# Kernel optimization log

Hardware: AMD Instinct MI355X
Metric: run time of the kernel (lower is better)

## Reference

```python
import jax, jax.numpy as jnp
import numpy as np

B, T, C = 16, 512, 1024
D, K, W = 4096, 128, 8


def _scatter_topk(a, k, use_values):
    """Top-k along last axis; return dense array with top-k values (or 1.0) scattered, zeros elsewhere."""
    shp = a.shape
    a2 = a.reshape(-1, shp[-1])
    vals, idx = jax.lax.top_k(a2, k)
    rows = jnp.arange(a2.shape[0])[:, None]
    src = vals if use_values else jnp.ones_like(vals)
    return jnp.zeros_like(a2).at[rows, idx].set(src).reshape(shp)


def _window_topk(x, k, window_size):
    # x: (B, T, D)
    b, t, d = x.shape
    stride = max(1, window_size // 2)
    if stride >= t:
        num_windows, pad, t_pad = 1, 0, t
    else:
        num_windows = (t - window_size) // stride + 1
        required = (num_windows - 1) * stride + window_size
        pad = max(0, required - t)
        t_pad = t + pad
    if pad > 0:
        x = jnp.pad(x, ((0, 0), (0, pad), (0, 0)))
    starts = jnp.arange(num_windows) * stride                      # (NW,)
    tidx = starts[:, None] + jnp.arange(window_size)               # (NW, W)
    x_windows = x[:, tidx, :]                                      # (B, NW, W, D)
    window_sums = x_windows.sum(axis=2)                            # (B, NW, D)
    mask_windows = _scatter_topk(window_sums, k, use_values=False)  # (B, NW, D)
    votes = (x_windows * mask_windows[:, :, None, :]).reshape(b, num_windows * window_size, d)
    feature_votes = jnp.zeros((b, t_pad, d), x.dtype).at[:, tidx.reshape(-1)].add(votes)
    mask_combined = _scatter_topk(feature_votes, k, use_values=False)  # (B, Tp, D)
    x_sparse = x * mask_combined
    return x_sparse[:, :t - 0, :] if pad > 0 else x_sparse


def setup_inputs() -> dict:
    key = jax.random.key(0)
    ks = jax.random.split(key, 4)
    x_ssl = jax.random.normal(ks[0], (B, T, C), jnp.float32)
    W_dec = jax.random.normal(ks[1], (C, D), jnp.float32)
    W_dec = W_dec / jnp.linalg.norm(W_dec, axis=0, keepdims=True)
    W_enc = W_dec.T                                                # tied init, as in module
    W1 = jax.random.normal(ks[2], (256, D), jnp.float32) * (1.0 / np.sqrt(D))
    W2 = jax.random.normal(ks[3], (2, 256), jnp.float32) * (1.0 / np.sqrt(256))
    return dict(
        x_ssl=x_ssl, W_enc=W_enc, b_enc=jnp.zeros((D,), jnp.float32),
        W_dec=W_dec, b_dec=jnp.zeros((C,), jnp.float32),
        ln_g=jnp.ones((D,), jnp.float32), ln_b=jnp.zeros((D,), jnp.float32),
        W1=W1, b1=jnp.zeros((256,), jnp.float32),
        W2=W2, b2=jnp.zeros((2,), jnp.float32),
    )


def reference(x_ssl, W_enc, b_enc, W_dec, b_dec, ln_g, ln_b, W1, b1, W2, b2):
    b, t, c = x_ssl.shape
    x_flat = x_ssl.reshape(b * t, c)
    # SAE encode with window top-k (window_size=8 > 1 path)
    pre = jnp.einsum('nc,dc->nd', x_flat - b_dec, W_enc) + b_enc
    post_relu = jax.nn.relu(pre).reshape(b, t, -1)                 # (B, T, D)
    encoded = _window_topk(post_relu, K, W)                        # (B, T, D)
    encoded_flat = encoded.reshape(b * t, -1)
    # SAE decode + reconstruction loss
    x_recon = jnp.einsum('nd,cd->nc', encoded_flat, W_dec) + b_dec
    sae_loss = jnp.mean((x_recon - x_flat) ** 2)
    # classifier on pooled sparse features (dropout is inference no-op)
    pooled = encoded.mean(axis=1)                                  # (B, D) == AdaptiveAvgPool1d(1)
    mu = pooled.mean(axis=-1, keepdims=True)
    var = pooled.var(axis=-1, keepdims=True)
    ln = (pooled - mu) / jnp.sqrt(var + 1e-5) * ln_g + ln_b
    h = jax.nn.relu(ln @ W1.T + b1)
    logits = h @ W2.T + b2
    log_probs = jax.nn.log_softmax(logits, axis=-1)
    return log_probs, sae_loss
```

## Files before the change

### kernel.cpp

```cpp
#include <hip/hip_runtime.h>

#define BB   16
#define TT   512
#define CC   1024
#define DD   4096
#define NN   (BB*TT)
#define NWIN 127
#define KTOP 128

typedef __attribute__((ext_vector_type(8))) short short8;
typedef _Float16 half8 __attribute__((ext_vector_type(8)));
typedef __attribute__((ext_vector_type(4))) float f32x4;

__device__ __forceinline__ unsigned short f2bf(float f) {
    unsigned u = __float_as_uint(f);
    unsigned r = (u + 0x7fffu + ((u >> 16) & 1u)) >> 16;
    return (unsigned short)r;
}
__device__ __forceinline__ float bf2f(unsigned x) {
    return __uint_as_float((x & 0xffffu) << 16);
}
__device__ __forceinline__ unsigned short f2h(float f) {
    union { _Float16 h; unsigned short u; } c;
    c.h = (_Float16)f;
    return c.u;
}
__device__ __forceinline__ unsigned tokey(float f) {
    unsigned u = __float_as_uint(f);
    return (u & 0x80000000u) ? ~u : (u | 0x80000000u);
}
__device__ __forceinline__ void async_lds16(const void* g, void* l) {
    __builtin_amdgcn_global_load_lds((const __attribute__((address_space(1))) void*)g,
                                     (__attribute__((address_space(3))) void*)l, 16, 0, 0);
}

__device__ __forceinline__ unsigned wave_prefix_incl(unsigned v) {
    int lane = threadIdx.x & 63;
#pragma unroll
    for (int off = 1; off < 64; off <<= 1) {
        unsigned n = __shfl_up(v, off, 64);
        if (lane >= off) v += n;
    }
    return v;
}
__device__ __forceinline__ unsigned wave_suffix_incl(unsigned v) {
    int lane = threadIdx.x & 63;
#pragma unroll
    for (int off = 1; off < 64; off <<= 1) {
        unsigned n = __shfl_down(v, off, 64);
        if (lane + off < 64) v += n;
    }
    return v;
}

__device__ __forceinline__ unsigned select_top128(const unsigned* keys,
                                                  unsigned* hist, unsigned* shx) {
    const int tid = threadIdx.x, wid = tid >> 6, lane = tid & 63;
    const unsigned ZKEY = 0x80000000u;
    unsigned cpos = 0, cz = 0;
#pragma unroll
    for (int i = 0; i < 16; ++i) {
        cpos += (keys[i] > ZKEY);
        cz   += (keys[i] == ZKEY);
    }
    unsigned ppos = wave_prefix_incl(cpos);
    unsigned pz   = wave_prefix_incl(cz);
    if (lane == 63) { shx[wid] = ppos; shx[4 + wid] = pz; }
    __syncthreads();
    unsigned nz = shx[0] + shx[1] + shx[2] + shx[3];
    unsigned selbits = 0u;
    if (nz <= KTOP) {
        unsigned need = KTOP - nz;
        unsigned zr = pz - cz;
        if (wid > 0) zr += shx[4];
        if (wid > 1) zr += shx[5];
        if (wid > 2) zr += shx[6];
#pragma unroll
        for (int i = 0; i < 16; ++i) {
            bool sel = (keys[i] > ZKEY) || (keys[i] == ZKEY && zr < need);
            if (keys[i] == ZKEY) ++zr;
            selbits |= (sel ? 1u : 0u) << i;
        }
        return selbits;
    }
    unsigned k2[16];
#pragma unroll
    for (int i = 0; i < 16; ++i) k2[i] = (keys[i] > ZKEY) ? keys[i] : 0u;
    unsigned prefix = 0u, pmask = 0u, Kr = KTOP;
    for (int shift = 24; shift >= 0; shift -= 8) {
        hist[tid] = 0u; hist[256 + tid] = 0u; hist[512 + tid] = 0u; hist[768 + tid] = 0u;
        __syncthreads();
        unsigned* h = hist + (wid << 8);
#pragma unroll
        for (int i = 0; i < 16; ++i)
            if (k2[i] && (k2[i] & pmask) == prefix) atomicAdd(&h[(k2[i] >> shift) & 255u], 1u);
        __syncthreads();
        unsigned v = hist[tid] + hist[256 + tid] + hist[512 + tid] + hist[768 + tid];
        unsigned s = wave_suffix_incl(v);
        if (lane == 0) shx[wid] = s;
        __syncthreads();
        unsigned stot = s;
        if (wid == 0) stot += shx[1] + shx[2] + shx[3];
        else if (wid == 1) stot += shx[2] + shx[3];
        else if (wid == 2) stot += shx[3];
        unsigned above = stot - v;
        if (stot >= Kr && above < Kr) { shx[8] = (unsigned)tid; shx[9] = Kr - above; }
        __syncthreads();
        prefix |= shx[8] << shift;
        pmask |= 0xFFu << shift;
        Kr = shx[9];
    }
    unsigned T = prefix, need = Kr;
    unsigned ce = 0;
#pragma unroll
    for (int i = 0; i < 16; ++i) ce += (k2[i] == T);
    unsigned pe = wave_prefix_incl(ce);
    __syncthreads();
    if (lane == 63) shx[4 + wid] = pe;
    __syncthreads();
    unsigned er = pe - ce;
    if (wid > 0) er += shx[4];
    if (wid > 1) er += shx[5];
    if (wid > 2) er += shx[6];
#pragma unroll
    for (int i = 0; i < 16; ++i) {
        bool sel = (k2[i] > T) || (k2[i] == T && er < need);
        if (k2[i] == T) ++er;
        selbits |= (sel ? 1u : 0u) << i;
    }
    return selbits;
}

__global__ __launch_bounds__(256) void k_convert(const float* __restrict__ in,
                                                 unsigned short* __restrict__ out,
                                                 size_t n4) {
    size_t i = (size_t)blockIdx.x * 256 + threadIdx.x;
    if (i >= n4) return;
    float4 v = ((const float4*)in)[i];
    uint2 o;
    o.x = (unsigned)f2bf(v.x) | ((unsigned)f2bf(v.y) << 16);
    o.y = (unsigned)f2bf(v.z) | ((unsigned)f2bf(v.w) << 16);
    ((uint2*)out)[i] = o;
}

__global__ __launch_bounds__(256) void k_convert_f16(const float* __restrict__ in,
                                                     unsigned short* __restrict__ out,
                                                     const float* __restrict__ bias,
                                                     size_t n4) {
    size_t i = (size_t)blockIdx.x * 256 + threadIdx.x;
    if (i >= n4) return;
    float4 v = ((const float4*)in)[i];
    if (bias) {
        size_t c = (i * 4) & (CC - 1);
        v.x -= bias[c]; v.y -= bias[c + 1]; v.z -= bias[c + 2]; v.w -= bias[c + 3];
    }
    uint2 o;
    o.x = (unsigned)f2h(v.x) | ((unsigned)f2h(v.y) << 16);
    o.y = (unsigned)f2h(v.z) | ((unsigned)f2h(v.w) << 16);
    ((uint2*)out)[i] = o;
}

__device__ __forceinline__ void stage_tile_swz(const unsigned short* gbase, size_t ldk,
                                               unsigned short* lds, int wave, int lane) {
    const int sub = lane >> 3;
    const int cj  = (lane & 7) ^ sub;
#pragma unroll
    for (int i = 0; i < 4; ++i) {
        int n = wave * 4 + i;
        int r = n * 8 + sub;
        async_lds16(gbase + (size_t)r * ldk + cj * 8, lds + n * 512);
    }
}

__global__ __launch_bounds__(256) void k_gemm_enc_f16(const unsigned short* __restrict__ Ah,
                                                      const unsigned short* __restrict__ Bh,
                                                      const float* __restrict__ bias,
                                                      float* __restrict__ Cout,
                                                      float* __restrict__ gsum,
                                                      int Ndim, int Kdim) {
    __shared__ __align__(16) unsigned short At[128 * 64];
    __shared__ __align__(16) unsigned short Bt[128 * 64];
    const int tid = threadIdx.x, wave = tid >> 6, lane = tid & 63;
    const int bm = blockIdx.y * 128, bn = blockIdx.x * 128;
    const int wm = (wave >> 1) * 64, wn = (wave & 1) * 64;
    const int rA = lane & 15, q8 = (lane >> 4) * 8, rp7 = rA & 7;
    f32x4 acc[4][4] = {};
    for (int k0 = 0; k0 < Kdim; k0 += 64) {
        __syncthreads();
        stage_tile_swz(Ah + (size_t)bm * Kdim + k0, Kdim, At, wave, lane);
        stage_tile_swz(Bh + (size_t)bn * Kdim + k0, Kdim, Bt, wave, lane);
        __syncthreads();
#pragma unroll
        for (int kk = 0; kk < 64; kk += 32) {
            const int sc = ((((kk + q8) >> 3) ^ rp7) << 3);
            half8 a[4], b[4];
#pragma unroll
            for (int mt = 0; mt < 4; ++mt) a[mt] = *(const half8*)(At + (wm + mt * 16 + rA) * 64 + sc);
#pragma unroll
            for (int nt = 0; nt < 4; ++nt) b[nt] = *(const half8*)(Bt + (wn + nt * 16 + rA) * 64 + sc);
#pragma unroll
            for (int mt = 0; mt < 4; ++mt)
#pragma unroll
                for (int nt = 0; nt < 4; ++nt)
                    acc[mt][nt] = __builtin_amdgcn_mfma_f32_16x16x32_f16(a[mt], b[nt], acc[mt][nt], 0, 0, 0);
        }
    }
    const int cl = lane & 15, qr = (lane >> 4) * 4;
#pragma unroll
    for (int nt = 0; nt < 4; ++nt) {
        int col = bn + wn + nt * 16 + cl;
        float bv = bias[col];
#pragma unroll
        for (int mt = 0; mt < 4; ++mt) {
            int row0 = bm + wm + mt * 16 + qr;
            float gs = 0.f;
#pragma unroll
            for (int r = 0; r < 4; ++r) {
                float v = acc[mt][nt][r] + bv;
                v = v > 0.f ? v : 0.f;
                gs += v;
                Cout[(size_t)(row0 + r) * Ndim + col] = v;
            }
            if (gsum) gsum[(size_t)(row0 >> 2) * Ndim + col] = gs;
        }
    }
}

__global__ __launch_bounds__(256) void k_gemm_recon(const unsigned short* __restrict__ A,
                                                    size_t lda,
                                                    const unsigned short* __restrict__ Bm,
                                                    const float* __restrict__ bdec,
                                                    const float* __restrict__ X,
                                                    float* __restrict__ sae,
                                                    int Ndim, int Kdim) {
    __shared__ __align__(16) unsigned short At[128 * 64];
    __shared__ __align__(16) unsigned short Bt[128 * 64];
    __shared__ float red[256];
    const int tid = threadIdx.x, wave = tid >> 6, lane = tid & 63;
    const int bm = blockIdx.y * 128, bn = blockIdx.x * 128;
    const int wm = (wave >> 1) * 64, wn = (wave & 1) * 64;
    const int rA = lane & 15, q8 = (lane >> 4) * 8, rp7 = rA & 7;
    f32x4 acc[4][4] = {};
    for (int k0 = 0; k0 < Kdim; k0 += 64) {
        __syncthreads();
        stage_tile_swz(A + (size_t)bm * lda + k0, lda, At, wave, lane);
        stage_tile_swz(Bm + (size_t)bn * Kdim + k0, Kdim, Bt, wave, lane);
        __syncthreads();
#pragma unroll
        for (int kk = 0; kk < 64; kk += 32) {
            const int sc = ((((kk + q8) >> 3) ^ rp7) << 3);
            short8 a[4], b[4];
#pragma unroll
            for (int mt = 0; mt < 4; ++mt) a[mt] = *(const short8*)(At + (wm + mt * 16 + rA) * 64 + sc);
#pragma unroll
            for (int nt = 0; nt < 4; ++nt) b[nt] = *(const short8*)(Bt + (wn + nt * 16 + rA) * 64 + sc);
#pragma unroll
            for (int mt = 0; mt < 4; ++mt)
#pragma unroll
                for (int nt = 0; nt < 4; ++nt)
                    acc[mt][nt] = __builtin_amdgcn_mfma_f32_16x16x32_bf16(a[mt], b[nt], acc[mt][nt], 0, 0, 0);
        }
    }
    const int cl = lane & 15, qr = (lane >> 4) * 4;
    float lsum = 0.f;
#pragma unroll
    for (int nt = 0; nt < 4; ++nt) {
        int col = bn + wn + nt * 16 + cl;
        float bv = bdec[col];
#pragma unroll
        for (int mt = 0; mt < 4; ++mt) {
            int row0 = bm + wm + mt * 16 + qr;
#pragma unroll
            for (int r = 0; r < 4; ++r) {
                float v = acc[mt][nt][r] + bv - X[(size_t)(row0 + r) * Ndim + col];
                lsum += v * v;
            }
        }
    }
    red[tid] = lsum;
    __syncthreads();
    for (int s = 128; s > 0; s >>= 1) { if (tid < s) red[tid] += red[tid + s]; __syncthreads(); }
    if (tid == 0) atomicAdd(sae, red[0]);
}

__global__ __launch_bounds__(256) void k_winsum_g(const float* __restrict__ gsum,
                                                  unsigned* __restrict__ wmask) {
    __shared__ unsigned hist[1024];
    __shared__ unsigned shx[16];
    __shared__ unsigned short halves[256];
    const int tid = threadIdx.x, w = blockIdx.x, b = blockIdx.y;
    const float* g0 = gsum + ((size_t)(b * 128 + w)) * DD + tid * 16;
    const float* g1 = g0 + DD;
    unsigned keys[16];
#pragma unroll
    for (int q = 0; q < 4; ++q) {
        float4 u = *(const float4*)(g0 + q * 4);
        float4 v = *(const float4*)(g1 + q * 4);
        keys[q * 4 + 0] = tokey(u.x + v.x);
        keys[q * 4 + 1] = tokey(u.y + v.y);
        keys[q * 4 + 2] = tokey(u.z + v.z);
        keys[q * 4 + 3] = tokey(u.w + v.w);
    }
    unsigned selbits = select_top128(keys, hist, shx);
    halves[tid] = (unsigned short)selbits;
    __syncthreads();
    if (tid < 128)
        wmask[(size_t)(b * NWIN + w) * 128 + tid] =
            (unsigned)halves[2 * tid] | ((unsigned)halves[2 * tid + 1] << 16);
}

__global__ __launch_bounds__(256) void k_winsum_p(const float* __restrict__ post,
                                                  unsigned* __restrict__ wmask) {
    __shared__ unsigned hist[1024];
    __shared__ unsigned shx[16];
    __shared__ unsigned short halves[256];
    const int tid = threadIdx.x, w = blockIdx.x, b = blockIdx.y;
    const float* base = post + (size_t)(b * TT + w * 4) * DD + tid * 16;
    float s[16] = {};
#pragma unroll
    for (int j = 0; j < 8; ++j) {
        const float* rp = base + (size_t)j * DD;
#pragma unroll
        for (int q = 0; q < 4; ++q) {
            float4 u = *(const float4*)(rp + q * 4);
            s[q * 4 + 0] += u.x; s[q * 4 + 1] += u.y; s[q * 4 + 2] += u.z; s[q * 4 + 3] += u.w;
        }
    }
    unsigned keys[16];
#pragma unroll
    for (int i = 0; i < 16; ++i) keys[i] = tokey(s[i]);
    unsigned selbits = select_top128(keys, hist, shx);
    halves[tid] = (unsigned short)selbits;
    __syncthreads();
    if (tid < 128)
        wmask[(size_t)(b * NWIN + w) * 128 + tid] =
            (unsigned)halves[2 * tid] | ((unsigned)halves[2 * tid + 1] << 16);
}

__global__ __launch_bounds__(256) void k_votes(float* __restrict__ post,
                                               const unsigned* __restrict__ wmask,
                                               float* __restrict__ pooled) {
    __shared__ unsigned hist[1024];
    __shared__ unsigned shx[16];
    const int tid = threadIdx.x, t = blockIdx.x, b = blockIdx.y;
    float* rp = post + (size_t)(b * TT + t) * DD;
    int w1 = t >> 2, w0 = w1 - 1;
    unsigned mw0 = 0u, mw1 = 0u;
    if (w0 >= 0)        mw0 = wmask[(size_t)(b * NWIN + w0) * 128 + (tid >> 1)];
    if (w1 <= NWIN - 1) mw1 = wmask[(size_t)(b * NWIN + w1) * 128 + (tid >> 1)];
    const int bbase = (tid & 1) * 16;
    float vals[16];
    unsigned keys[16];
#pragma unroll
    for (int q = 0; q < 4; ++q) {
        float4 u = *(const float4*)(rp + tid * 16 + q * 4);
        vals[q * 4 + 0] = u.x; vals[q * 4 + 1] = u.y; vals[q * 4 + 2] = u.z; vals[q * 4 + 3] = u.w;
    }
#pragma unroll
    for (int i = 0; i < 16; ++i) {
        float cov = (float)(((mw0 >> (bbase + i)) & 1u) + ((mw1 >> (bbase + i)) & 1u));
        keys[i] = tokey(vals[i] * cov);
    }
    unsigned selbits = select_top128(keys, hist, shx);
    unsigned packed[8];
#pragma unroll
    for (int i = 0; i < 16; i += 2) {
        float v0 = (selbits >> i) & 1u ? vals[i] : 0.f;
        float v1 = (selbits >> (i + 1)) & 1u ? vals[i + 1] : 0.f;
        if (v0 != 0.f) atomicAdd(&pooled[(size_t)b * DD + tid * 16 + i], v0);
        if (v1 != 0.f) atomicAdd(&pooled[(size_t)b * DD + tid * 16 + i + 1], v1);
        packed[i >> 1] = (unsigned)f2bf(v0) | ((unsigned)f2bf(v1) << 16);
    }
    unsigned short* op = (unsigned short*)rp;
    *(uint4*)(op + tid * 16)     = *(uint4*)&packed[0];
    *(uint4*)(op + tid * 16 + 8) = *(uint4*)&packed[4];
}

__device__ __forceinline__ float block_sum(float v, float* red) {
    const int tid = threadIdx.x;
    red[tid] = v;
    __syncthreads();
    for (int s = 128; s > 0; s >>= 1) { if (tid < s) red[tid] += red[tid + s]; __syncthreads(); }
    float r = red[0];
    __syncthreads();
    return r;
}

__global__ __launch_bounds__(256) void k_head_ln(const float* __restrict__ pooled,
                                                 const float* __restrict__ lng,
                                                 const float* __restrict__ lnb,
                                                 float* __restrict__ lnout) {
    __shared__ float red[256];
    const int b = blockIdx.x, tid = threadIdx.x;
    float pv[16];
    float s = 0.f;
#pragma unroll
    for (int q = 0; q < 4; ++q) {
        float4 u = *(const float4*)(pooled + (size_t)b * DD + tid * 16 + q * 4);
        pv[q * 4 + 0] = u.x * (1.f / TT); pv[q * 4 + 1] = u.y * (1.f / TT);
        pv[q * 4 + 2] = u.z * (1.f / TT); pv[q * 4 + 3] = u.w * (1.f / TT);
        s += pv[q * 4 + 0] + pv[q * 4 + 1] + pv[q * 4 + 2] + pv[q * 4 + 3];
    }
    float mean = block_sum(s, red) * (1.f / (float)DD);
    float vs = 0.f;
#pragma unroll
    for (int i = 0; i < 16; ++i) { float c = pv[i] - mean; vs += c * c; }
    float var = block_sum(vs, red) * (1.f / (float)DD);
    float inv = rsqrtf(var + 1e-5f);
#pragma unroll
    for (int q = 0; q < 4; ++q) {
        float4 g = *(const float4*)(lng + tid * 16 + q * 4);
        float4 bb = *(const float4*)(lnb + tid * 16 + q * 4);
        float4 o;
        o.x = (pv[q * 4 + 0] - mean) * inv * g.x + bb.x;
        o.y = (pv[q * 4 + 1] - mean) * inv * g.y + bb.y;
        o.z = (pv[q * 4 + 2] - mean) * inv * g.z + bb.z;
        o.w = (pv[q * 4 + 3] - mean) * inv * g.w + bb.w;
        *(float4*)(lnout + (size_t)b * DD + tid * 16 + q * 4) = o;
    }
}

__global__ __launch_bounds__(256) void k_head_mlp(const float* __restrict__ lnout,
                                                  const float* __restrict__ W1,
                                                  const float* __restrict__ b1,
                                                  float* __restrict__ h) {
    const int gw = (blockIdx.x * 256 + threadIdx.x) >> 6;
    const int lane = threadIdx.x & 63;
    const int b = gw >> 8, row = gw & 255;
    const float* lp = lnout + (size_t)b * DD;
    const float* wr = W1 + (size_t)row * DD;
    float a = 0.f;
#pragma unroll
    for (int k = 0; k < DD / 64; ++k)
        a += lp[lane + 64 * k] * wr[lane + 64 * k];
#pragma unroll
    for (int off = 32; off > 0; off >>= 1) a += __shfl_down(a, off, 64);
    if (lane == 0) h[b * 256 + row] = fmaxf(a + b1[row], 0.f);
}

__global__ __launch_bounds__(256) void k_head_out(const float* __restrict__ h,
                                                  const float* __restrict__ W2,
                                                  const float* __restrict__ b2,
                                                  const float* __restrict__ sae,
                                                  float* __restrict__ out) {
    __shared__ float red[256];
    const int b = blockIdx.x, tid = threadIdx.x;
    float hv = h[b * 256 + tid];
    float l0 = block_sum(hv * W2[tid], red) + b2[0];
    float l1 = block_sum(hv * W2[256 + tid], red) + b2[1];
    if (tid == 0) {
        float m = fmaxf(l0, l1);
        float lse = m + logf(expf(l0 - m) + expf(l1 - m));
        out[2 * b] = l0 - lse;
        out[2 * b + 1] = l1 - lse;
        if (b == 0) out[32] = sae[0] * (1.f / (float)((size_t)NN * CC));
    }
}

extern "C" void kernel_launch(void* const* d_in, const int* in_sizes, int n_in,
                              void* d_out, int out_size, void* d_ws, size_t ws_size,
                              hipStream_t stream) {
    const float* x    = (const float*)d_in[0];
    const float* Wenc = (const float*)d_in[1];
    const float* benc = (const float*)d_in[2];
    const float* Wdec = (const float*)d_in[3];
    const float* bdec = (const float*)d_in[4];
    const float* lng  = (const float*)d_in[5];
    const float* lnb  = (const float*)d_in[6];
    const float* W1   = (const float*)d_in[7];
    const float* b1   = (const float*)d_in[8];
    const float* W2   = (const float*)d_in[9];
    const float* b2   = (const float*)d_in[10];
    float* out = (float*)d_out;

    char* ws = (char*)d_ws;
    float*          post  = (float*)(ws + 0);
    unsigned short* xh16  = (unsigned short*)(ws + 134217728);
    unsigned short* scr   = (unsigned short*)(ws + 150994944);
    unsigned short* wh16  = (unsigned short*)(ws + 167772160);
    unsigned short* wdecb = (unsigned short*)(ws + 184549376);
    unsigned*       wmask = (unsigned*)(ws + 192937984);
    float*          pooled= (float*)(ws + 193978368);
    float*          sae   = (float*)(ws + 194240512);
    float*          gsum  = (float*)(ws + 194240768);
    const bool use_gsum = ws_size >= (size_t)194240768 + 33554432;
    float* gptr = use_gsum ? gsum : nullptr;
    float* lnout = (float*)xh16;
    float* hbuf  = (float*)scr;

    hipMemsetAsync(pooled, 0, 262144 + 256, stream);

    k_convert_f16<<<dim3((NN * CC) / 1024), 256, 0, stream>>>(x, xh16, bdec, (size_t)NN * CC / 4);
    k_convert_f16<<<dim3((DD * CC) / 1024), 256, 0, stream>>>(Wenc, wh16, nullptr, (size_t)DD * CC / 4);
    k_convert<<<dim3((CC * DD) / 1024), 256, 0, stream>>>(Wdec, wdecb, (size_t)CC * DD / 4);

    k_gemm_enc_f16<<<dim3(DD / 128, NN / 128), 256, 0, stream>>>(xh16, wh16, benc, post, gptr, DD, CC);
    if (use_gsum)
        k_winsum_g<<<dim3(NWIN, BB), 256, 0, stream>>>(gsum, wmask);
    else
        k_winsum_p<<<dim3(NWIN, BB), 256, 0, stream>>>(post, wmask);
    k_votes<<<dim3(TT, BB), 256, 0, stream>>>(post, wmask, pooled);
    k_gemm_recon<<<dim3(CC / 128, NN / 128), 256, 0, stream>>>((const unsigned short*)post, (size_t)2 * DD,
                                                               wdecb, bdec, x, sae, CC, DD);
    k_head_ln<<<dim3(BB), 256, 0, stream>>>(pooled, lng, lnb, lnout);
    k_head_mlp<<<dim3(1024), 256, 0, stream>>>(lnout, W1, b1, hbuf);
    k_head_out<<<dim3(BB), 256, 0, stream>>>(hbuf, W2, b2, sae, out);
}
```

Measured before the change: 468.8 us.

## Fuse conversions, stage encoder epilogue through LDS, double-buffer recon GEMM

```diff
diff --git a/kernel.cpp b/kernel.cpp
--- a/kernel.cpp
+++ b/kernel.cpp
@@ -131,33 +131,38 @@
     return selbits;
 }
 
-__global__ __launch_bounds__(256) void k_convert(const float* __restrict__ in,
-                                                 unsigned short* __restrict__ out,
-                                                 size_t n4) {
-    size_t i = (size_t)blockIdx.x * 256 + threadIdx.x;
-    if (i >= n4) return;
-    float4 v = ((const float4*)in)[i];
-    uint2 o;
-    o.x = (unsigned)f2bf(v.x) | ((unsigned)f2bf(v.y) << 16);
-    o.y = (unsigned)f2bf(v.z) | ((unsigned)f2bf(v.w) << 16);
-    ((uint2*)out)[i] = o;
-}
-
-__global__ __launch_bounds__(256) void k_convert_f16(const float* __restrict__ in,
-                                                     unsigned short* __restrict__ out,
-                                                     const float* __restrict__ bias,
-                                                     size_t n4) {
-    size_t i = (size_t)blockIdx.x * 256 + threadIdx.x;
-    if (i >= n4) return;
-    float4 v = ((const float4*)in)[i];
-    if (bias) {
+__global__ __launch_bounds__(256) void k_convert_all(const float* __restrict__ x,
+                                                     const float* __restrict__ Wenc,
+                                                     const float* __restrict__ Wdec,
+                                                     const float* __restrict__ bdec,
+                                                     unsigned short* __restrict__ xh,
+                                                     unsigned short* __restrict__ wh,
+                                                     unsigned short* __restrict__ wdb) {
+    const int bid = blockIdx.x;
+    if (bid < 8192) {
+        size_t i = (size_t)bid * 256 + threadIdx.x;
+        float4 v = ((const float4*)x)[i];
         size_t c = (i * 4) & (CC - 1);
-        v.x -= bias[c]; v.y -= bias[c + 1]; v.z -= bias[c + 2]; v.w -= bias[c + 3];
-    }
-    uint2 o;
-    o.x = (unsigned)f2h(v.x) | ((unsigned)f2h(v.y) << 16);
-    o.y = (unsigned)f2h(v.z) | ((unsigned)f2h(v.w) << 16);
-    ((uint2*)out)[i] = o;
+        v.x -= bdec[c]; v.y -= bdec[c + 1]; v.z -= bdec[c + 2]; v.w -= bdec[c + 3];
+        uint2 o;
+        o.x = (unsigned)f2h(v.x) | ((unsigned)f2h(v.y) << 16);
+        o.y = (unsigned)f2h(v.z) | ((unsigned)f2h(v.w) << 16);
+        ((uint2*)xh)[i] = o;
+    } else if (bid < 12288) {
+        size_t i = (size_t)(bid - 8192) * 256 + threadIdx.x;
+        float4 v = ((const float4*)Wenc)[i];
+        uint2 o;
+        o.x = (unsigned)f2h(v.x) | ((unsigned)f2h(v.y) << 16);
+        o.y = (unsigned)f2h(v.z) | ((unsigned)f2h(v.w) << 16);
+        ((uint2*)wh)[i] = o;
+    } else {
+        size_t i = (size_t)(bid - 12288) * 256 + threadIdx.x;
+        float4 v = ((const float4*)Wdec)[i];
+        uint2 o;
+        o.x = (unsigned)f2bf(v.x) | ((unsigned)f2bf(v.y) << 16);
+        o.y = (unsigned)f2bf(v.z) | ((unsigned)f2bf(v.w) << 16);
+        ((uint2*)wdb)[i] = o;
+    }
 }
 
 __device__ __forceinline__ void stage_tile_swz(const unsigned short* gbase, size_t ldk,
@@ -178,12 +183,15 @@
                                                       float* __restrict__ Cout,
                                                       float* __restrict__ gsum,
                                                       int Ndim, int Kdim) {
-    __shared__ __align__(16) unsigned short At[128 * 64];
-    __shared__ __align__(16) unsigned short Bt[128 * 64];
+    __shared__ __align__(16) unsigned short smem[2 * 128 * 64];
+    unsigned short* At = smem;
+    unsigned short* Bt = smem + 128 * 64;
+    float* cbuf = (float*)smem;
     const int tid = threadIdx.x, wave = tid >> 6, lane = tid & 63;
     const int bm = blockIdx.y * 128, bn = blockIdx.x * 128;
     const int wm = (wave >> 1) * 64, wn = (wave & 1) * 64;
     const int rA = lane & 15, q8 = (lane >> 4) * 8, rp7 = rA & 7;
+    const int q = lane >> 4, qr = q * 4, cl = lane & 15;
     f32x4 acc[4][4] = {};
     for (int k0 = 0; k0 < Kdim; k0 += 64) {
         __syncthreads();
@@ -205,23 +213,46 @@
                     acc[mt][nt] = __builtin_amdgcn_mfma_f32_16x16x32_f16(a[mt], b[nt], acc[mt][nt], 0, 0, 0);
         }
     }
-    const int cl = lane & 15, qr = (lane >> 4) * 4;
-#pragma unroll
-    for (int nt = 0; nt < 4; ++nt) {
-        int col = bn + wn + nt * 16 + cl;
-        float bv = bias[col];
-#pragma unroll
-        for (int mt = 0; mt < 4; ++mt) {
-            int row0 = bm + wm + mt * 16 + qr;
-            float gs = 0.f;
-#pragma unroll
-            for (int r = 0; r < 4; ++r) {
-                float v = acc[mt][nt][r] + bv;
-                v = v > 0.f ? v : 0.f;
-                gs += v;
-                Cout[(size_t)(row0 + r) * Ndim + col] = v;
+    float bv[4];
+#pragma unroll
+    for (int nt = 0; nt < 4; ++nt) bv[nt] = bias[bn + wn + nt * 16 + cl];
+#pragma unroll
+    for (int p = 0; p < 2; ++p) {
+        __syncthreads();
+        if ((wave >> 1) == p) {
+#pragma unroll
+            for (int nt = 0; nt < 4; ++nt) {
+                int lc = wn + nt * 16 + cl;
+                int pcb = (lc >> 2) ^ (q << 1);
+#pragma unroll
+                for (int mt = 0; mt < 4; ++mt) {
+#pragma unroll
+                    for (int r = 0; r < 4; ++r) {
+                        int lr = mt * 16 + qr + r;
+                        float v = acc[mt][nt][r] + bv[nt];
+                        v = v > 0.f ? v : 0.f;
+                        cbuf[lr * 128 + pcb * 4 + (lc & 3)] = v;
+                    }
+                }
             }
-            if (gsum) gsum[(size_t)(row0 >> 2) * Ndim + col] = gs;
+        }
+        __syncthreads();
+#pragma unroll
+        for (int i = 0; i < 2; ++i) {
+            int gidx = i * 256 + tid;
+            int grow = gidx >> 5;
+            int colg = gidx & 31;
+            float4 s = make_float4(0.f, 0.f, 0.f, 0.f);
+#pragma unroll
+            for (int j = 0; j < 4; ++j) {
+                int lr = grow * 4 + j;
+                int pcr = colg ^ (((lr >> 2) & 3) << 1);
+                float4 v = *(const float4*)&cbuf[lr * 128 + pcr * 4];
+                s.x += v.x; s.y += v.y; s.z += v.z; s.w += v.w;
+                *(float4*)&Cout[(size_t)(bm + p * 64 + lr) * Ndim + bn + colg * 4] = v;
+            }
+            if (gsum)
+                *(float4*)&gsum[(size_t)((bm >> 2) + p * 16 + grow) * Ndim + bn + colg * 4] = s;
         }
     }
 }
@@ -233,33 +264,38 @@
                                                     const float* __restrict__ X,
                                                     float* __restrict__ sae,
                                                     int Ndim, int Kdim) {
-    __shared__ __align__(16) unsigned short At[128 * 64];
-    __shared__ __align__(16) unsigned short Bt[128 * 64];
+    __shared__ __align__(16) unsigned short At[2][128 * 64];
+    __shared__ __align__(16) unsigned short Bt[2][128 * 64];
     __shared__ float red[256];
     const int tid = threadIdx.x, wave = tid >> 6, lane = tid & 63;
     const int bm = blockIdx.y * 128, bn = blockIdx.x * 128;
     const int wm = (wave >> 1) * 64, wn = (wave & 1) * 64;
     const int rA = lane & 15, q8 = (lane >> 4) * 8, rp7 = rA & 7;
     f32x4 acc[4][4] = {};
+    stage_tile_swz(A + (size_t)bm * lda, lda, At[0], wave, lane);
+    stage_tile_swz(Bm + (size_t)bn * Kdim, Kdim, Bt[0], wave, lane);
+    __syncthreads();
     for (int k0 = 0; k0 < Kdim; k0 += 64) {
-        __syncthreads();
-        stage_tile_swz(A + (size_t)bm * lda + k0, lda, At, wave, lane);
-        stage_tile_swz(Bm + (size_t)bn * Kdim + k0, Kdim, Bt, wave, lane);
-        __syncthreads();
+        const int cur = (k0 >> 6) & 1;
+        if (k0 + 64 < Kdim) {
+            stage_tile_swz(A + (size_t)bm * lda + k0 + 64, lda, At[cur ^ 1], wave, lane);
+            stage_tile_swz(Bm + (size_t)bn * Kdim + k0 + 64, Kdim, Bt[cur ^ 1], wave, lane);
+        }
 #pragma unroll
         for (int kk = 0; kk < 64; kk += 32) {
             const int sc = ((((kk + q8) >> 3) ^ rp7) << 3);
             short8 a[4], b[4];
 #pragma unroll
-            for (int mt = 0; mt < 4; ++mt) a[mt] = *(const short8*)(At + (wm + mt * 16 + rA) * 64 + sc);
-#pragma unroll
-            for (int nt = 0; nt < 4; ++nt) b[nt] = *(const short8*)(Bt + (wn + nt * 16 + rA) * 64 + sc);
+            for (int mt = 0; mt < 4; ++mt) a[mt] = *(const short8*)(At[cur] + (wm + mt * 16 + rA) * 64 + sc);
+#pragma unroll
+            for (int nt = 0; nt < 4; ++nt) b[nt] = *(const short8*)(Bt[cur] + (wn + nt * 16 + rA) * 64 + sc);
 #pragma unroll
             for (int mt = 0; mt < 4; ++mt)
 #pragma unroll
                 for (int nt = 0; nt < 4; ++nt)
                     acc[mt][nt] = __builtin_amdgcn_mfma_f32_16x16x32_bf16(a[mt], b[nt], acc[mt][nt], 0, 0, 0);
         }
+        __syncthreads();
     }
     const int cl = lane & 15, qr = (lane >> 4) * 4;
     float lsum = 0.f;
@@ -490,9 +526,7 @@
 
     hipMemsetAsync(pooled, 0, 262144 + 256, stream);
 
-    k_convert_f16<<<dim3((NN * CC) / 1024), 256, 0, stream>>>(x, xh16, bdec, (size_t)NN * CC / 4);
-    k_convert_f16<<<dim3((DD * CC) / 1024), 256, 0, stream>>>(Wenc, wh16, nullptr, (size_t)DD * CC / 4);
-    k_convert<<<dim3((CC * DD) / 1024), 256, 0, stream>>>(Wdec, wdecb, (size_t)CC * DD / 4);
+    k_convert_all<<<dim3(16384), 256, 0, stream>>>(x, Wenc, Wdec, bdec, xh16, wh16, wdecb);
 
     k_gemm_enc_f16<<<dim3(DD / 128, NN / 128), 256, 0, stream>>>(xh16, wh16, benc, post, gptr, DD, CC);
     if (use_gsum)
```

New measurement: 454.0 us. 3.2% less time.
